# Optimization experiments

Hardware: AMD Instinct MI355X
Metric: run time of the kernel (lower is better)

Reference implementation:

```python
import jax, jax.numpy as jnp
import numpy as np

S, B, H, Dh = 3072, 1, 16, 64

def setup_inputs() -> dict:
    key = jax.random.key(0)
    kq, kk, kv, km = jax.random.split(key, 4)
    query = jax.random.normal(kq, (S, B, H, Dh), dtype=jnp.float32)
    key_t = jax.random.normal(kk, (S, B, H, Dh), dtype=jnp.float32)
    value = jax.random.normal(kv, (S, B, H, Dh), dtype=jnp.float32)
    attention_mask = jax.random.randint(km, (1, 1, S, S), 0, 2).astype(bool)  # True = keep
    return {"query": query, "key": key_t, "value": value,
            "attention_mask": attention_mask, "attn_mask_type": 0}

def reference(query, key, value, attention_mask, attn_mask_type):
    # sbhd -> bshd
    q = jnp.transpose(query, (1, 0, 2, 3))   # (B,Sq,H,D)
    k = jnp.transpose(key,   (1, 0, 2, 3))   # (B,Sk,H,D)
    v = jnp.transpose(value, (1, 0, 2, 3))   # (B,Sk,H,D)
    scale = 1.0 / jnp.sqrt(jnp.asarray(q.shape[-1], q.dtype))
    scores = jnp.einsum('bqhd,bkhd->bhqk', q, k) * scale  # (B,H,Sq,Sk)
    scores = jnp.where(attention_mask, scores, -jnp.inf)  # bool mask, True=keep
    attn = jax.nn.softmax(scores, axis=-1)
    out = jnp.einsum('bhqk,bkhd->bqhd', attn, v)           # (B,Sq,H,D)
    return out
```

## Files before the change

### kernel.cpp

```cpp
#include <hip/hip_runtime.h>
#include <stdint.h>

#define SEQ 3072
#define NH  16
#define DH  64
#define WQ  32
#define KVBLK 64
#define NKT (SEQ / KVBLK)
#define NQT (SEQ / WQ)
#define NWORDS (SEQ * SEQ / 64)

typedef __attribute__((ext_vector_type(8))) __bf16 bf16x8;
typedef __attribute__((ext_vector_type(16))) float f32x16;

union BF8 { ushort us[8]; uint u[4]; uint4 u4; bf16x8 v; };

__device__ __forceinline__ ushort f2bf(float f) {
    uint u = __builtin_bit_cast(uint, f);
    return (ushort)((u + 0x7FFFu + ((u >> 16) & 1u)) >> 16);
}

__global__ void detect_kernel(const uint32_t* __restrict__ m, int* __restrict__ flag) {
    __shared__ int cntA, cntB;
    if (threadIdx.x == 0) { cntA = 0; cntB = 0; }
    __syncthreads();
    int a = 0, b = 0;
    for (int i = 0; i < 16; ++i) {
        uint32_t w = m[threadIdx.x + i * 256];
        if (w & 0xFFFFFF00u) a = 1;
        if (w & 0x0000FFFFu) b = 1;
    }
    if (a) atomicOr(&cntA, 1);
    if (b) atomicOr(&cntB, 1);
    __syncthreads();
    if (threadIdx.x == 0) *flag = (cntA == 0) ? 1 : ((cntB == 0) ? 2 : 0);
}

__global__ void pack_kernel(const void* __restrict__ mask, const int* __restrict__ flag,
                            uint64_t* __restrict__ bits) {
    int g = blockIdx.x * 256 + threadIdx.x;
    int f = *flag;
    bool v;
    if (f == 1)      v = ((const int*)mask)[g] != 0;
    else if (f == 2) v = ((const float*)mask)[g] != 0.0f;
    else             v = ((const unsigned char*)mask)[g] != 0;
    uint64_t b = __ballot(v);
    if ((threadIdx.x & 63) == 0) {
        int w = g >> 6;
        int qrow = w / NKT, cw = w % NKT;
        bits[(size_t)cw * SEQ + qrow] = b;
    }
}

#define SCALE_Q (0.125f * 1.44269504f)
__global__ void convert_q(const float* __restrict__ Q, ushort* __restrict__ Qb) {
    int i = (blockIdx.x * 256 + threadIdx.x) * 8;
    float4 a = *(const float4*)(Q + i);
    float4 b = *(const float4*)(Q + i + 4);
    BF8 t;
    t.us[0] = f2bf(a.x * SCALE_Q); t.us[1] = f2bf(a.y * SCALE_Q);
    t.us[2] = f2bf(a.z * SCALE_Q); t.us[3] = f2bf(a.w * SCALE_Q);
    t.us[4] = f2bf(b.x * SCALE_Q); t.us[5] = f2bf(b.y * SCALE_Q);
    t.us[6] = f2bf(b.z * SCALE_Q); t.us[7] = f2bf(b.w * SCALE_Q);
    *(uint4*)(Qb + i) = t.u4;
}

__global__ __launch_bounds__(256)
void convert_kv(const float* __restrict__ K, const float* __restrict__ V,
                ushort* __restrict__ Kbz, ushort* __restrict__ Vtz) {
    const int kt = blockIdx.x, h = blockIdx.y;
    const int tid = threadIdx.x;
    __shared__ float Vf[64][68];

    {
        const int kr = tid >> 2, dc = (tid & 3) * 16;
        const float* vsrc = V + (((size_t)(kt * KVBLK + kr) * NH + h) * DH + dc);
        #pragma unroll
        for (int j = 0; j < 4; ++j) {
            float4 t = *(const float4*)(vsrc + 4 * j);
            Vf[kr][dc + 4 * j + 0] = t.x; Vf[kr][dc + 4 * j + 1] = t.y;
            Vf[kr][dc + 4 * j + 2] = t.z; Vf[kr][dc + 4 * j + 3] = t.w;
        }
    }

    ushort* kout = Kbz + ((size_t)(h * NKT + kt)) * 4096;
    #pragma unroll
    for (int i = 0; i < 2; ++i) {
        const int idx = tid + 256 * i;
        const int f = idx >> 6, l = idx & 63;
        const int kc = f >> 1, kh = f & 1;
        const int row = kh * 32 + (l & 31);
        const int kcol = kc * 16 + (l >> 5) * 8;
        const float* ks = K + (((size_t)(kt * KVBLK + row) * NH + h) * DH + kcol);
        float4 a = *(const float4*)(ks);
        float4 b = *(const float4*)(ks + 4);
        BF8 t;
        t.us[0] = f2bf(a.x); t.us[1] = f2bf(a.y); t.us[2] = f2bf(a.z); t.us[3] = f2bf(a.w);
        t.us[4] = f2bf(b.x); t.us[5] = f2bf(b.y); t.us[6] = f2bf(b.z); t.us[7] = f2bf(b.w);
        *(uint4*)(kout + idx * 8) = t.u4;
    }

    __syncthreads();

    ushort* vout = Vtz + ((size_t)(h * NKT + kt)) * 4096;
    #pragma unroll
    for (int i = 0; i < 2; ++i) {
        const int idx = tid + 256 * i;
        const int f = idx >> 6, l = idx & 63;
        const int kc = f >> 1, dh = f & 1;
        const int d = dh * 32 + (l & 31);
        const int kr0 = kc * 16 + (l >> 5) * 8;
        BF8 t;
        #pragma unroll
        for (int j = 0; j < 8; ++j)
            t.us[j] = f2bf(Vf[kr0 + j][d]);
        *(uint4*)(vout + idx * 8) = t.u4;
    }
}

__device__ __forceinline__ bf16x8 ldfrag(const ushort* tile, int f, int lane) {
    return *(const bf16x8*)(tile + f * 512 + lane * 8);
}

__device__ __forceinline__ void process_tile(
    const bf16x8 kf[8], const bf16x8 vf[8], const bf16x8 qf[4],
    uint64_t mw, int hh, f32x16& o0, f32x16& o1, float& l_)
{
    const uint64_t mu = mw >> (4 * hh);
    const uint mlo = (uint)mu, mhi = (uint)(mu >> 32);
    f32x16 s0, s1;
    #pragma unroll
    for (int r = 0; r < 16; ++r) {
        const int sh = (r & 3) + 8 * (r >> 2);
        const uint b0 = (mlo >> sh) & 1u;
        const uint b1 = (mhi >> sh) & 1u;
        s0[r] = __builtin_bit_cast(float, (b0 - 1u) & 0xFF800000u);
        s1[r] = __builtin_bit_cast(float, (b1 - 1u) & 0xFF800000u);
    }

    __builtin_amdgcn_s_setprio(1);
    #pragma unroll
    for (int kc = 0; kc < 4; ++kc) {
        s0 = __builtin_amdgcn_mfma_f32_32x32x16_bf16(kf[kc * 2 + 0], qf[kc], s0, 0, 0, 0);
        s1 = __builtin_amdgcn_mfma_f32_32x32x16_bf16(kf[kc * 2 + 1], qf[kc], s1, 0, 0, 0);
    }
    __builtin_amdgcn_s_setprio(0);

    float la0 = 0.f, la1 = 0.f;
    #pragma unroll
    for (int r = 0; r < 16; ++r) {
        float p0 = __builtin_amdgcn_exp2f(s0[r]);
        float p1 = __builtin_amdgcn_exp2f(s1[r]);
        s0[r] = p0; s1[r] = p1;
        la0 += p0; la1 += p1;
    }
    l_ += la0 + la1;

    bf16x8 pa[4];
    {
        #define PKSWAP(dlo, dhi, a0, a1, b0, b1)                                   \
            {   uint wl, wh;                                                       \
                asm("v_cvt_pk_bf16_f32 %0, %1, %2" : "=v"(wl) : "v"(a0), "v"(a1)); \
                asm("v_cvt_pk_bf16_f32 %0, %1, %2" : "=v"(wh) : "v"(b0), "v"(b1)); \
                asm("v_permlane32_swap_b32 %0, %1" : "+v"(wl), "+v"(wh));          \
                dlo = wl; dhi = wh; }
        BF8 t0, t1, t2, t3;
        PKSWAP(t0.u[0], t0.u[2], s0[0],  s0[1],  s0[4],  s0[5]);
        PKSWAP(t0.u[1], t0.u[3], s0[2],  s0[3],  s0[6],  s0[7]);
        PKSWAP(t1.u[0], t1.u[2], s0[8],  s0[9],  s0[12], s0[13]);
        PKSWAP(t1.u[1], t1.u[3], s0[10], s0[11], s0[14], s0[15]);
        PKSWAP(t2.u[0], t2.u[2], s1[0],  s1[1],  s1[4],  s1[5]);
        PKSWAP(t2.u[1], t2.u[3], s1[2],  s1[3],  s1[6],  s1[7]);
        PKSWAP(t3.u[0], t3.u[2], s1[8],  s1[9],  s1[12], s1[13]);
        PKSWAP(t3.u[1], t3.u[3], s1[10], s1[11], s1[14], s1[15]);
        pa[0] = t0.v; pa[1] = t1.v; pa[2] = t2.v; pa[3] = t3.v;
        #undef PKSWAP
    }

    __builtin_amdgcn_s_setprio(1);
    #pragma unroll
    for (int kc = 0; kc < 4; ++kc) {
        o0 = __builtin_amdgcn_mfma_f32_32x32x16_bf16(pa[kc], vf[kc * 2 + 0], o0, 0, 0, 0);
        o1 = __builtin_amdgcn_mfma_f32_32x32x16_bf16(pa[kc], vf[kc * 2 + 1], o1, 0, 0, 0);
    }
    __builtin_amdgcn_s_setprio(0);
}

__global__ __launch_bounds__(256, 2)
void attn12(const ushort* __restrict__ Qb, const ushort* __restrict__ Kbz,
            const ushort* __restrict__ Vtz, const uint64_t* __restrict__ bits2,
            float* __restrict__ out)
{
    const int bid = blockIdx.x;
    const int swz = (bid & 7) * 48 + (bid >> 3);
    const int h = swz / 24, qg = swz % 24;
    const int tid = threadIdx.x;
    const int wv = tid >> 6, lane = tid & 63;
    const int lq = lane & 31, hh = lane >> 5;
    const int qt = qg * 4 + wv;
    const int qrow0 = qt * WQ;

    bf16x8 qf[4];
    {
        const ushort* qp = Qb + ((size_t)(qrow0 + lq) * NH + h) * DH;
        #pragma unroll
        for (int kc = 0; kc < 4; ++kc)
            qf[kc] = *(const bf16x8*)(qp + kc * 16 + hh * 8);
    }

    f32x16 o0, o1;
    #pragma unroll
    for (int i = 0; i < 16; ++i) { o0[i] = 0.f; o1[i] = 0.f; }
    float l_ = 0.f;

    const ushort* kbase = Kbz + (size_t)h * NKT * 4096;
    const ushort* vbase = Vtz + (size_t)h * NKT * 4096;
    const uint64_t* bb = bits2 + qrow0 + lq;

    bf16x8 kA[8], kB[8], vC[8];

    #pragma unroll
    for (int f = 0; f < 8; ++f) kA[f] = ldfrag(kbase, f, lane);
    uint64_t mwA = bb[0];

    for (int it = 0; it < NKT; it += 2) {
        {
            const ushort* vt = vbase + (size_t)it * 4096;
            #pragma unroll
            for (int f = 0; f < 8; ++f) vC[f] = ldfrag(vt, f, lane);
            const ushort* kn = kbase + (size_t)(it + 1) * 4096;
            #pragma unroll
            for (int f = 0; f < 8; ++f) kB[f] = ldfrag(kn, f, lane);
            const uint64_t mwB = bb[(size_t)(it + 1) * SEQ];
            process_tile(kA, vC, qf, mwA, hh, o0, o1, l_);
            mwA = mwB;
        }
        {
            const int t2 = (it + 2 < NKT) ? it + 2 : NKT - 1;
            const ushort* vt = vbase + (size_t)(it + 1) * 4096;
            #pragma unroll
            for (int f = 0; f < 8; ++f) vC[f] = ldfrag(vt, f, lane);
            const ushort* kn = kbase + (size_t)t2 * 4096;
            #pragma unroll
            for (int f = 0; f < 8; ++f) kA[f] = ldfrag(kn, f, lane);
            const uint64_t mwN = bb[(size_t)t2 * SEQ];
            process_tile(kB, vC, qf, mwA, hh, o0, o1, l_);
            mwA = mwN;
        }
    }

    {
        float a = l_, b = l_;
        asm("v_permlane32_swap_b32 %0, %1" : "+v"(a), "+v"(b));
        l_ = a + b;
    }
    const float inv = (l_ > 0.f) ? 1.0f / l_ : 0.f;
    #pragma unroll
    for (int r = 0; r < 16; ++r) {
        const int q_r = (r & 3) + 8 * (r >> 2) + 4 * hh;
        const float ir = __shfl(inv, q_r);
        float* op = out + ((size_t)(qrow0 + q_r) * NH + h) * DH;
        op[lq]      = o0[r] * ir;
        op[lq + 32] = o1[r] * ir;
    }
}

__global__ __launch_bounds__(256, 2)
void attn_fb(const float* __restrict__ Q, const float* __restrict__ K,
             const float* __restrict__ V, const int* __restrict__ mask_i32,
             float* __restrict__ out)
{
    const int qtile = blockIdx.x, h = blockIdx.y;
    const int tid  = threadIdx.x;
    const int wv   = tid >> 6, lane = tid & 63;
    const int g    = lane >> 4, c = lane & 15;
    const int qb   = qtile * 64 + wv * 16;

    typedef __attribute__((ext_vector_type(4))) float f32x4;
    __shared__ __align__(16) ushort KbS[KVBLK * 72];
    __shared__ __align__(16) ushort VtS[DH * 72];
    __shared__ __align__(16) ushort PbS[4 * 16 * 72];
    ushort* Pw = &PbS[wv * 16 * 72];

    bf16x8 qa[2];
    {
        const float* qp = Q + ((qb + c) * NH + h) * DH;
        #pragma unroll
        for (int kk = 0; kk < 2; ++kk) {
            BF8 t;
            const float4* pp = (const float4*)(qp + kk * 32 + g * 8);
            float4 f0 = pp[0], f1 = pp[1];
            t.us[0] = f2bf(f0.x * 0.125f); t.us[1] = f2bf(f0.y * 0.125f);
            t.us[2] = f2bf(f0.z * 0.125f); t.us[3] = f2bf(f0.w * 0.125f);
            t.us[4] = f2bf(f1.x * 0.125f); t.us[5] = f2bf(f1.y * 0.125f);
            t.us[6] = f2bf(f1.z * 0.125f); t.us[7] = f2bf(f1.w * 0.125f);
            qa[kk] = t.v;
        }
    }

    f32x4 oacc[4];
    float m_[4], lsum[4];
    #pragma unroll
    for (int nt = 0; nt < 4; ++nt) oacc[nt] = (f32x4){0.f, 0.f, 0.f, 0.f};
    #pragma unroll
    for (int r = 0; r < 4; ++r) { m_[r] = -1e30f; lsum[r] = 0.f; }

    const int srow0 = tid >> 3;
    const int fch   = tid & 7;

    for (int kt = 0; kt < NKT; ++kt) {
        __syncthreads();
        #pragma unroll
        for (int i = 0; i < 2; ++i) {
            const int krow = srow0 + 32 * i;
            const int gofs = ((kt * KVBLK + krow) * NH + h) * DH + fch * 8;
            const float4* kp = (const float4*)(K + gofs);
            const float4* vp = (const float4*)(V + gofs);
            float4 k0 = kp[0], k1 = kp[1];
            float4 v0 = vp[0], v1 = vp[1];
            BF8 kb;
            kb.us[0] = f2bf(k0.x); kb.us[1] = f2bf(k0.y);
            kb.us[2] = f2bf(k0.z); kb.us[3] = f2bf(k0.w);
            kb.us[4] = f2bf(k1.x); kb.us[5] = f2bf(k1.y);
            kb.us[6] = f2bf(k1.z); kb.us[7] = f2bf(k1.w);
            *(uint4*)&KbS[krow * 72 + (fch ^ (krow & 7)) * 8] = kb.u4;
            float vf[8] = {v0.x, v0.y, v0.z, v0.w, v1.x, v1.y, v1.z, v1.w};
            #pragma unroll
            for (int j = 0; j < 8; ++j) {
                const int d = fch * 8 + j;
                VtS[d * 72 + ((krow >> 3) ^ ((d >> 3) & 7)) * 8 + (krow & 7)] = f2bf(vf[j]);
            }
        }
        __syncthreads();

        f32x4 sacc[4];
        #pragma unroll
        for (int nt = 0; nt < 4; ++nt) sacc[nt] = (f32x4){0.f, 0.f, 0.f, 0.f};
        #pragma unroll
        for (int kk = 0; kk < 2; ++kk) {
            #pragma unroll
            for (int nt = 0; nt < 4; ++nt) {
                const int krow = nt * 16 + c;
                bf16x8 kf = *(const bf16x8*)&KbS[krow * 72 + (((g + 4 * kk) ^ (krow & 7))) * 8];
                sacc[nt] = __builtin_amdgcn_mfma_f32_16x16x32_bf16(qa[kk], kf, sacc[nt], 0, 0, 0);
            }
        }

        float pmax[4];
        #pragma unroll
        for (int r = 0; r < 4; ++r) pmax[r] = -1e30f;
        #pragma unroll
        for (int nt = 0; nt < 4; ++nt) {
            #pragma unroll
            for (int r = 0; r < 4; ++r) {
                bool keep = mask_i32[(size_t)(qb + 4 * g + r) * SEQ + kt * KVBLK + nt * 16 + c] != 0;
                float s = keep ? sacc[nt][r] : -1e30f;
                sacc[nt][r] = s;
                pmax[r] = fmaxf(pmax[r], s);
            }
        }
        #pragma unroll
        for (int r = 0; r < 4; ++r) {
            float v = pmax[r];
            v = fmaxf(v, __shfl_xor(v, 1));
            v = fmaxf(v, __shfl_xor(v, 2));
            v = fmaxf(v, __shfl_xor(v, 4));
            v = fmaxf(v, __shfl_xor(v, 8));
            float nm = fmaxf(m_[r], v);
            float alpha = __expf(m_[r] - nm);
            m_[r] = nm;
            lsum[r] *= alpha;
            #pragma unroll
            for (int nt = 0; nt < 4; ++nt) oacc[nt][r] *= alpha;
        }
        #pragma unroll
        for (int nt = 0; nt < 4; ++nt) {
            #pragma unroll
            for (int r = 0; r < 4; ++r) {
                float pv = __expf(sacc[nt][r] - m_[r]);
                lsum[r] += pv;
                const int row = 4 * g + r, col = nt * 16 + c;
                Pw[row * 72 + (((col >> 3) ^ (row & 7))) * 8 + (col & 7)] = f2bf(pv);
            }
        }
        #pragma unroll
        for (int kk = 0; kk < 2; ++kk) {
            bf16x8 pa = *(const bf16x8*)&Pw[c * 72 + (((g + 4 * kk) ^ (c & 7))) * 8];
            #pragma unroll
            for (int nt = 0; nt < 4; ++nt) {
                const int d = nt * 16 + c;
                bf16x8 vb = *(const bf16x8*)&VtS[d * 72 + (((g + 4 * kk) ^ ((d >> 3) & 7))) * 8];
                oacc[nt] = __builtin_amdgcn_mfma_f32_16x16x32_bf16(pa, vb, oacc[nt], 0, 0, 0);
            }
        }
    }

    #pragma unroll
    for (int r = 0; r < 4; ++r) {
        float v = lsum[r];
        v += __shfl_xor(v, 1); v += __shfl_xor(v, 2);
        v += __shfl_xor(v, 4); v += __shfl_xor(v, 8);
        lsum[r] = (v > 0.f) ? 1.0f / v : 0.f;
    }
    #pragma unroll
    for (int nt = 0; nt < 4; ++nt) {
        #pragma unroll
        for (int r = 0; r < 4; ++r) {
            out[((qb + 4 * g + r) * NH + h) * DH + nt * 16 + c] = oacc[nt][r] * lsum[r];
        }
    }
}

extern "C" void kernel_launch(void* const* d_in, const int* in_sizes, int n_in,
                              void* d_out, int out_size, void* d_ws, size_t ws_size,
                              hipStream_t stream) {
    const float* Q    = (const float*)d_in[0];
    const float* K    = (const float*)d_in[1];
    const float* V    = (const float*)d_in[2];
    const void*  mask = d_in[3];
    float* out = (float*)d_out;

    const size_t off_bits = 64;
    const size_t off_qb   = off_bits + (size_t)NWORDS * 8;
    const size_t off_kbz  = off_qb  + (size_t)SEQ * NH * DH * 2;
    const size_t off_vtz  = off_kbz + (size_t)SEQ * NH * DH * 2;
    const size_t need     = off_vtz + (size_t)SEQ * NH * DH * 2;

    if (ws_size >= need) {
        int*      flag = (int*)d_ws;
        uint64_t* bits = (uint64_t*)((char*)d_ws + off_bits);
        ushort*   Qb   = (ushort*)((char*)d_ws + off_qb);
        ushort*   Kbz  = (ushort*)((char*)d_ws + off_kbz);
        ushort*   Vtz  = (ushort*)((char*)d_ws + off_vtz);
        detect_kernel<<<1, 256, 0, stream>>>((const uint32_t*)mask, flag);
        pack_kernel<<<SEQ * SEQ / 256, 256, 0, stream>>>(mask, flag, bits);
        convert_q<<<SEQ * NH * DH / (256 * 8), 256, 0, stream>>>(Q, Qb);
        convert_kv<<<dim3(NKT, NH), 256, 0, stream>>>(K, V, Kbz, Vtz);
        attn12<<<NQT * NH / 4, 256, 0, stream>>>(Qb, Kbz, Vtz, bits, out);
    } else {
        attn_fb<<<dim3(NKT, NH), 256, 0, stream>>>(Q, K, V, (const int*)mask, out);
    }
}
```

Baseline: 105.5 us.

## Split KV range across wave pairs and merge partial outputs via LDS

Each block now handles two 32-row query tiles, with two waves per tile each processing half of the KV sequence. The partial outputs and row sums of the second half are written to shared memory and merged by the first wave before normalisation. The grid doubles to 768 blocks and launch bounds target 4 blocks per CU, aiming to raise parallelism and occupancy and to shorten each wave's serial KV loop. The cost is an extra LDS round trip, a block-wide barrier, and half the waves sitting idle during the final store.

```diff
diff --git a/kernel.cpp b/kernel.cpp
--- a/kernel.cpp
+++ b/kernel.cpp
@@ -7,6 +7,7 @@
 #define WQ  32
 #define KVBLK 64
 #define NKT (SEQ / KVBLK)
+#define HALF_T (NKT / 2)
 #define NQT (SEQ / WQ)
 #define NWORDS (SEQ * SEQ / 64)
 
@@ -186,19 +187,21 @@
     __builtin_amdgcn_s_setprio(0);
 }
 
-__global__ __launch_bounds__(256, 2)
-void attn12(const ushort* __restrict__ Qb, const ushort* __restrict__ Kbz,
+__global__ __launch_bounds__(256, 4)
+void attn13(const ushort* __restrict__ Qb, const ushort* __restrict__ Kbz,
             const ushort* __restrict__ Vtz, const uint64_t* __restrict__ bits2,
             float* __restrict__ out)
 {
     const int bid = blockIdx.x;
-    const int swz = (bid & 7) * 48 + (bid >> 3);
-    const int h = swz / 24, qg = swz % 24;
+    const int swz = (bid & 7) * 96 + (bid >> 3);
+    const int h = swz / 48, qg = swz % 48;
     const int tid = threadIdx.x;
     const int wv = tid >> 6, lane = tid & 63;
+    const int qsub = wv & 1, kvh = wv >> 1;
     const int lq = lane & 31, hh = lane >> 5;
-    const int qt = qg * 4 + wv;
-    const int qrow0 = qt * WQ;
+    const int qrow0 = (qg * 2 + qsub) * WQ;
+
+    __shared__ __align__(16) float MergeF[2][2368];
 
     bf16x8 qf[4];
     {
@@ -213,9 +216,10 @@
     for (int i = 0; i < 16; ++i) { o0[i] = 0.f; o1[i] = 0.f; }
     float l_ = 0.f;
 
-    const ushort* kbase = Kbz + (size_t)h * NKT * 4096;
-    const ushort* vbase = Vtz + (size_t)h * NKT * 4096;
-    const uint64_t* bb = bits2 + qrow0 + lq;
+    const int kt0 = kvh * HALF_T;
+    const ushort* kbase = Kbz + ((size_t)(h * NKT + kt0)) * 4096;
+    const ushort* vbase = Vtz + ((size_t)(h * NKT + kt0)) * 4096;
+    const uint64_t* bb = bits2 + (size_t)kt0 * SEQ + qrow0 + lq;
 
     bf16x8 kA[8], kB[8], vC[8];
 
@@ -223,7 +227,7 @@
     for (int f = 0; f < 8; ++f) kA[f] = ldfrag(kbase, f, lane);
     uint64_t mwA = bb[0];
 
-    for (int it = 0; it < NKT; it += 2) {
+    for (int it = 0; it < HALF_T; it += 2) {
         {
             const ushort* vt = vbase + (size_t)it * 4096;
             #pragma unroll
@@ -236,7 +240,7 @@
             mwA = mwB;
         }
         {
-            const int t2 = (it + 2 < NKT) ? it + 2 : NKT - 1;
+            const int t2 = (it + 2 < HALF_T) ? it + 2 : HALF_T - 1;
             const ushort* vt = vbase + (size_t)(it + 1) * 4096;
             #pragma unroll
             for (int f = 0; f < 8; ++f) vC[f] = ldfrag(vt, f, lane);
@@ -254,14 +258,32 @@
         asm("v_permlane32_swap_b32 %0, %1" : "+v"(a), "+v"(b));
         l_ = a + b;
     }
-    const float inv = (l_ > 0.f) ? 1.0f / l_ : 0.f;
-    #pragma unroll
-    for (int r = 0; r < 16; ++r) {
-        const int q_r = (r & 3) + 8 * (r >> 2) + 4 * hh;
-        const float ir = __shfl(inv, q_r);
-        float* op = out + ((size_t)(qrow0 + q_r) * NH + h) * DH;
-        op[lq]      = o0[r] * ir;
-        op[lq + 32] = o1[r] * ir;
+
+    float* LMq = &MergeF[qsub][0];
+    if (kvh == 1) {
+        if (hh == 0) LMq[64 * 36 + lq] = l_;
+        #pragma unroll
+        for (int j = 0; j < 4; ++j) {
+            float4 t0, t1;
+            t0.x = o0[4 * j]; t0.y = o0[4 * j + 1]; t0.z = o0[4 * j + 2]; t0.w = o0[4 * j + 3];
+            t1.x = o1[4 * j]; t1.y = o1[4 * j + 1]; t1.z = o1[4 * j + 2]; t1.w = o1[4 * j + 3];
+            *(float4*)&LMq[lq * 36 + 4 * hh + 8 * j]        = t0;
+            *(float4*)&LMq[(lq + 32) * 36 + 4 * hh + 8 * j] = t1;
+        }
+    }
+    __syncthreads();
+    if (kvh == 0) {
+        const float lB = LMq[64 * 36 + lq];
+        const float l = l_ + lB;
+        const float inv = (l > 0.f) ? 1.0f / l : 0.f;
+        #pragma unroll
+        for (int r = 0; r < 16; ++r) {
+            const int q_r = (r & 3) + 8 * (r >> 2) + 4 * hh;
+            const float ir = __shfl(inv, q_r);
+            float* op = out + ((size_t)(qrow0 + q_r) * NH + h) * DH;
+            op[lq]      = (o0[r] + LMq[lq * 36 + q_r]) * ir;
+            op[lq + 32] = (o1[r] + LMq[(lq + 32) * 36 + q_r]) * ir;
+        }
     }
 }
 
@@ -436,7 +458,7 @@
         pack_kernel<<<SEQ * SEQ / 256, 256, 0, stream>>>(mask, flag, bits);
         convert_q<<<SEQ * NH * DH / (256 * 8), 256, 0, stream>>>(Q, Qb);
         convert_kv<<<dim3(NKT, NH), 256, 0, stream>>>(K, V, Kbz, Vtz);
-        attn12<<<NQT * NH / 4, 256, 0, stream>>>(Qb, Kbz, Vtz, bits, out);
+        attn13<<<NQT * NH / 2, 256, 0, stream>>>(Qb, Kbz, Vtz, bits, out);
     } else {
         attn_fb<<<dim3(NKT, NH), 256, 0, stream>>>(Q, K, V, (const int*)mask, out);
     }
```

After: 360.7 us. 242% more time.
